# Kernel optimization log

Hardware: AMD Instinct MI355X
Metric: run time of the kernel (lower is better)

Reference implementation:

```python
import math
import jax, jax.numpy as jnp
import numpy as np

B, S, D, H, DFF = 4, 2048, 1024, 16, 4096
DK = D // H
EPS = 1e-6


def setup_inputs() -> dict:
    key = jax.random.key(0)
    ks = jax.random.split(key, 12)
    w = lambda k, sh: jax.random.normal(k, sh, dtype=jnp.float32) * 0.02
    return {
        "x": jax.random.normal(ks[0], (B, S, D), dtype=jnp.float32),
        "mask": jax.random.randint(ks[1], (B, 1, S, S), 0, 2, dtype=jnp.int32),
        "ln1_a": jnp.ones((D,), jnp.float32), "ln1_b": jnp.zeros((D,), jnp.float32),
        "Wq": w(ks[2], (D, D)), "bq": jnp.zeros((D,), jnp.float32),
        "Wk": w(ks[3], (D, D)), "bk": jnp.zeros((D,), jnp.float32),
        "Wv": w(ks[4], (D, D)), "bv": jnp.zeros((D,), jnp.float32),
        "Wo": w(ks[5], (D, D)), "bo": jnp.zeros((D,), jnp.float32),
        "ln2_a": jnp.ones((D,), jnp.float32), "ln2_b": jnp.zeros((D,), jnp.float32),
        "W1": w(ks[6], (D, DFF)), "b1": jnp.zeros((DFF,), jnp.float32),
        "W2": w(ks[7], (DFF, D)), "b2": jnp.zeros((D,), jnp.float32),
    }


def layernorm(x, a, b):
    # BERT4REC LayerNorm: unbiased std (ddof=1), eps added to std (not var)
    mean = jnp.mean(x, axis=-1, keepdims=True)
    std = jnp.std(x, axis=-1, keepdims=True, ddof=1)
    return a * (x - mean) / (std + EPS) + b


def gelu_tanh(x):
    c = math.sqrt(2.0 / math.pi)
    return 0.5 * x * (1.0 + jnp.tanh(c * (x + 0.044715 * x * x * x)))


def reference(x, mask, ln1_a, ln1_b, Wq, bq, Wk, bk, Wv, bv, Wo, bo,
              ln2_a, ln2_b, W1, b1, W2, b2):
    xb = layernorm(x, ln1_a, ln1_b)
    # multi-head attention (dropout off / eval mode)
    q = (xb @ Wq + bq).reshape(B, S, H, DK).transpose(0, 2, 1, 3)
    k = (xb @ Wk + bk).reshape(B, S, H, DK).transpose(0, 2, 1, 3)
    v = (xb @ Wv + bv).reshape(B, S, H, DK).transpose(0, 2, 1, 3)
    scores = jnp.einsum("bhqd,bhkd->bhqk", q, k) / math.sqrt(DK)
    scores = jnp.where(mask == 0, jnp.float32(-1e9), scores)
    p = jax.nn.softmax(scores, axis=-1)
    attn = jnp.einsum("bhqk,bhkd->bhqd", p, v)
    attn = attn.transpose(0, 2, 1, 3).reshape(B, S, D)
    x = x + (attn @ Wo + bo)
    # FFN sublayer
    xb = layernorm(x, ln2_a, ln2_b)
    ff = gelu_tanh(xb @ W1 + b1) @ W2 + b2
    return x + ff
```

## Files before the change

kernel.cpp:

```cpp
#include <hip/hip_runtime.h>

#define Bb 4
#define Ss 2048
#define Dd 1024
#define Hh 16
#define DFF 4096

typedef unsigned short u16;
typedef __attribute__((ext_vector_type(8))) short v8s;
typedef __attribute__((ext_vector_type(4))) float v4f;
typedef __attribute__((ext_vector_type(4))) unsigned short v4u16;
typedef __attribute__((ext_vector_type(4))) unsigned v4u;

__device__ __forceinline__ u16 f2bf(float f) {
  unsigned u = __builtin_bit_cast(unsigned, f);
  return (u16)((u + 0x7fffu + ((u >> 16) & 1u)) >> 16);
}

__device__ __forceinline__ unsigned cvtpk(float a, float b) {
  unsigned r;
  asm("v_cvt_pk_bf16_f32 %0, %1, %2" : "=v"(r) : "v"(a), "v"(b));
  return r;
}

__device__ __forceinline__ void gload16(const void* g, void* l) {
  __builtin_amdgcn_global_load_lds((const __attribute__((address_space(1))) unsigned*)g,
                                   (__attribute__((address_space(3))) unsigned*)l, 16, 0, 0);
}

__device__ __forceinline__ v4f mfma16(v8s a, v8s b, v4f c) {
  return __builtin_amdgcn_mfma_f32_16x16x32_bf16(a, b, c, 0, 0, 0);
}

__device__ __forceinline__ float gelu_f(float x) {
  float y = 0.7978845608028654f * (x + 0.044715f * x * x * x);
  y = fminf(fmaxf(y, -15.f), 15.f);
  float t = 1.0f - 2.0f / (__expf(2.0f * y) + 1.0f);
  return 0.5f * x * (1.0f + t);
}

__global__ __launch_bounds__(256)
void ln_k(const float* __restrict__ x, const float* __restrict__ ga,
          const float* __restrict__ gb, u16* __restrict__ out) {
  const int row = blockIdx.x, tid = threadIdx.x;
  const float4 v = ((const float4*)(x + (size_t)row * 1024))[tid];
  float s = v.x + v.y + v.z + v.w;
  float q = v.x * v.x + v.y * v.y + v.z * v.z + v.w * v.w;
  #pragma unroll
  for (int o = 1; o < 64; o <<= 1) { s += __shfl_xor(s, o); q += __shfl_xor(q, o); }
  __shared__ float red[8];
  if ((tid & 63) == 0) { red[tid >> 6] = s; red[4 + (tid >> 6)] = q; }
  __syncthreads();
  s = red[0] + red[1] + red[2] + red[3];
  q = red[4] + red[5] + red[6] + red[7];
  const float mean = s * (1.0f / 1024.0f);
  const float var = fmaxf((q - 1024.0f * mean * mean) * (1.0f / 1023.0f), 0.0f);
  const float inv = 1.0f / (sqrtf(var) + 1e-6f);
  const int c0 = tid * 4;
  u16* o4 = out + (size_t)row * 1024 + c0;
  const float vv[4] = {v.x, v.y, v.z, v.w};
  #pragma unroll
  for (int i = 0; i < 4; i++)
    o4[i] = f2bf(ga[c0 + i] * (vv[i] - mean) * inv + gb[c0 + i]);
}

__global__ __launch_bounds__(256)
void wt_k(const float* __restrict__ w, u16* __restrict__ wt, int K, int N) {
  __shared__ float tile[32 * 33];
  const int t = threadIdx.x;
  const int k0 = blockIdx.x << 5, n0 = blockIdx.y << 5;
  {
    const int r = t >> 3, c4 = (t & 7) << 2;
    const float4 v = *(const float4*)&w[(size_t)(k0 + r) * N + n0 + c4];
    tile[r * 33 + c4 + 0] = v.x; tile[r * 33 + c4 + 1] = v.y;
    tile[r * 33 + c4 + 2] = v.z; tile[r * 33 + c4 + 3] = v.w;
  }
  __syncthreads();
  {
    const int r = t >> 3, c4 = (t & 7) << 2;
    v4u16 uv;
    #pragma unroll
    for (int i = 0; i < 4; i++) uv[i] = f2bf(tile[(c4 + i) * 33 + r]);
    *(v4u16*)&wt[(size_t)(n0 + r) * K + k0 + c4] = uv;
  }
}

__global__ void bcat_k(const float* bq, const float* bk, const float* bv, float* dst) {
  int i = blockIdx.x * 256 + threadIdx.x;
  dst[i] = i < 1024 ? bq[i] : (i < 2048 ? bk[i - 1024] : bv[i - 2048]);
}

__global__ __launch_bounds__(256)
void mask_k(const int* __restrict__ mask, unsigned* __restrict__ mw) {
  const size_t w = (size_t)blockIdx.x * 256 + threadIdx.x;
  const int4* p = (const int4*)(mask + w * 32);
  unsigned bits = 0;
  #pragma unroll
  for (int k = 0; k < 8; k++) {
    const int4 v = p[k];
    bits |= (v.x != 0 ? 1u : 0u) << (k * 4 + 0);
    bits |= (v.y != 0 ? 1u : 0u) << (k * 4 + 1);
    bits |= (v.z != 0 ? 1u : 0u) << (k * 4 + 2);
    bits |= (v.w != 0 ? 1u : 0u) << (k * 4 + 3);
  }
  mw[w] = bits;
}

__global__ __launch_bounds__(256)
void vt_k(const u16* __restrict__ qkv, u16* __restrict__ vt) {
  __shared__ __align__(16) u16 tile[64 * 72];
  const int t = threadIdx.x;
  const int bh = blockIdx.y, b = bh >> 4, h = bh & 15;
  const size_t s0 = (size_t)blockIdx.x * 64;
  {
    const int row = t >> 2, c0 = (t & 3) << 4;
    const u16* src = &qkv[((size_t)b * Ss + s0 + row) * 3072 + 2048 + h * 64 + c0];
    *(v8s*)&tile[row * 72 + c0] = *(const v8s*)src;
    *(v8s*)&tile[row * 72 + c0 + 8] = *(const v8s*)(src + 8);
  }
  __syncthreads();
  {
    const int dk = t >> 2, sc0 = (t & 3) << 4;
    u16* dst = &vt[((size_t)bh * 64 + dk) * Ss + s0 + sc0];
    v4u16 a, bvv, cvv, d;
    #pragma unroll
    for (int i = 0; i < 4; i++) a[i] = tile[(sc0 + i) * 72 + dk];
    #pragma unroll
    for (int i = 0; i < 4; i++) bvv[i] = tile[(sc0 + 4 + i) * 72 + dk];
    #pragma unroll
    for (int i = 0; i < 4; i++) cvv[i] = tile[(sc0 + 8 + i) * 72 + dk];
    #pragma unroll
    for (int i = 0; i < 4; i++) d[i] = tile[(sc0 + 12 + i) * 72 + dk];
    *(v4u16*)(dst + 0) = a; *(v4u16*)(dst + 4) = bvv;
    *(v4u16*)(dst + 8) = cvv; *(v4u16*)(dst + 12) = d;
  }
}

template<int EPI>
__global__ __launch_bounds__(256)
void gemm_bt(const u16* __restrict__ A, const u16* __restrict__ Bt,
             const float* __restrict__ bias, const float* res,
             void* out, int M, int N, int K) {
  __shared__ __align__(16) u16 lA[2][128 * 32];
  __shared__ __align__(16) u16 lB[2][128 * 32];
  const int tid = threadIdx.x;
  const int lane = tid & 63, wid = tid >> 6;
  const int c = lane & 15, g = lane >> 4;
  const int nt = N >> 7;
  const int nwg = gridDim.x;
  const int bid0 = blockIdx.x;
  const int bid = (bid0 & 7) * (nwg >> 3) + (bid0 >> 3);
  const int bm = bid / nt, bn = bid - bm * nt;
  const int row0 = bm << 7, col0 = bn << 7;
  const int wr = (wid >> 1) << 6, wc = (wid & 1) << 6;

  v4f acc[4][4] = {};

  const int arow = tid >> 2, ak = (tid & 3) << 3;
  const u16* gA = A + (size_t)(row0 + arow) * K + ak;
  const u16* gB = Bt + (size_t)(col0 + arow) * K + ak;
  const int ldo = wid * 512;
  const size_t rstep = (size_t)64 * K;

  for (int kt = 0; kt < K; kt += 64) {
    __syncthreads();
    #pragma unroll
    for (int s = 0; s < 2; s++) {
      const int ks = kt + s * 32;
      gload16(gA + ks, &lA[s][ldo]);
      gload16(gA + ks + rstep, &lA[s][ldo + 2048]);
      gload16(gB + ks, &lB[s][ldo]);
      gload16(gB + ks + rstep, &lB[s][ldo + 2048]);
    }
    __syncthreads();
    #pragma unroll
    for (int s = 0; s < 2; s++) {
      v8s af[4], bfr[4];
      #pragma unroll
      for (int m = 0; m < 4; m++) af[m] = *(const v8s*)&lA[s][(wr + m * 16 + c) * 32 + g * 8];
      #pragma unroll
      for (int n = 0; n < 4; n++) bfr[n] = *(const v8s*)&lB[s][(wc + n * 16 + c) * 32 + g * 8];
      #pragma unroll
      for (int m = 0; m < 4; m++)
        #pragma unroll
        for (int n = 0; n < 4; n++)
          acc[m][n] = mfma16(af[m], bfr[n], acc[m][n]);
    }
  }

  float bv[4];
  #pragma unroll
  for (int n = 0; n < 4; n++) bv[n] = bias[col0 + wc + n * 16 + c];
  #pragma unroll
  for (int m = 0; m < 4; m++) {
    #pragma unroll
    for (int n = 0; n < 4; n++) {
      #pragma unroll
      for (int j = 0; j < 4; j++) {
        const int r = row0 + wr + m * 16 + g * 4 + j;
        const int cc = col0 + wc + n * 16 + c;
        const size_t idx = (size_t)r * N + cc;
        const float v = acc[m][n][j] + bv[n];
        if constexpr (EPI == 0) ((u16*)out)[idx] = f2bf(v);
        else if constexpr (EPI == 1) ((float*)out)[idx] = res[idx] + v;
        else ((u16*)out)[idx] = f2bf(gelu_f(v));
      }
    }
  }
}

__global__ __launch_bounds__(256, 4)
void attn_k(const u16* __restrict__ qkv, const u16* __restrict__ vt,
            const unsigned* __restrict__ mw, u16* __restrict__ ctx) {
  __shared__ __align__(16) u16 lK[128 * 64];
  __shared__ __align__(16) u16 lV[64 * 128];

  const int tid = threadIdx.x, lane = tid & 63, wid = tid >> 6;
  const int c = lane & 15, g = lane >> 4;
  const bool b4 = (lane & 16) != 0;
  const int bid = blockIdx.x;
  const int swz = (bid & 7) * 128 + (bid >> 3);
  const int bh = swz >> 4, qb = swz & 15;
  const int b = bh >> 4, h = bh & 15;
  const int qw = (qb << 7) + wid * 32;

  v8s qs[2][2];
  #pragma unroll
  for (int m = 0; m < 2; m++)
    #pragma unroll
    for (int ks = 0; ks < 2; ks++) {
      const v8s q = *(const v8s*)&qkv[((size_t)b * Ss + qw + m * 16 + c) * 3072 + h * 64 + ks * 32 + g * 8];
      v4u w;
      #pragma unroll
      for (int p = 0; p < 4; p++) {
        const float a = __builtin_bit_cast(float, (unsigned)((u16)q[2 * p]) << 16) * 0.18033688f;
        const float e = __builtin_bit_cast(float, (unsigned)((u16)q[2 * p + 1]) << 16) * 0.18033688f;
        w[p] = cvtpk(a, e);
      }
      qs[m][ks] = __builtin_bit_cast(v8s, w);
    }

  v4f o[2][4] = {};
  float ls[2] = {0.f, 0.f};

  const unsigned* mrow0 = mw + ((size_t)b * Ss + qw + c) * 64;

  const int skey = tid >> 3;
  const int kchunk = (((tid & 7) ^ ((tid >> 3) & 7)) << 3);
  const int vdk = tid >> 4;
  const int vchunk = (((tid & 15) ^ ((tid >> 4) & 15)) << 3);
  const u16* gK = &qkv[((size_t)b * Ss + skey) * 3072 + 1024 + h * 64 + kchunk];
  const u16* gV = &vt[((size_t)bh * 64 + vdk) * Ss + vchunk];
  u16* const dK = &lK[(wid * 8) * 64];
  u16* const dV = &lV[(wid * 4) * 128];

  for (int kt = 0; kt < 16; kt++) {
    __syncthreads();
    #pragma unroll
    for (int i = 0; i < 4; i++) {
      gload16(gK + ((size_t)kt * 128 + i * 32) * 3072, dK + i * (32 * 64));
      gload16(gV + (size_t)(i * 16) * Ss + kt * 128, dV + i * (16 * 128));
    }
    __syncthreads();

    #pragma unroll
    for (int m = 0; m < 2; m++) {
      v4f sc[8] = {};
      #pragma unroll
      for (int f = 0; f < 8; f++) {
        const v8s k0 = *(const v8s*)&lK[(f * 16 + c) * 64 + ((g ^ (c & 7)) << 3)];
        const v8s k1 = *(const v8s*)&lK[(f * 16 + c) * 64 + (((g + 4) ^ (c & 7)) << 3)];
        sc[f] = mfma16(k0, qs[m][0], sc[f]);
        sc[f] = mfma16(k1, qs[m][1], sc[f]);
      }
      const uint4 mv = *(const uint4*)(mrow0 + (size_t)m * 16 * 64 + kt * 4);
      const unsigned mvw[4] = {mv.x, mv.y, mv.z, mv.w};
      float rs = 0.f;
      #pragma unroll
      for (int f = 0; f < 8; f++) {
        const unsigned bits = mvw[f >> 1] >> (((f & 1) << 4) + (g << 2));
        #pragma unroll
        for (int j = 0; j < 4; j++) {
          float p = exp2f(fminf(sc[f][j], 30.0f));
          p = ((bits >> j) & 1u) ? p : 0.0f;
          sc[f][j] = p;
          rs += p;
        }
      }
      rs += __shfl_xor(rs, 16);
      rs += __shfl_xor(rs, 32);
      ls[m] += rs;
      unsigned p0[8], p1[8];
      #pragma unroll
      for (int f = 0; f < 8; f++) {
        p0[f] = cvtpk(sc[f][0], sc[f][1]);
        p1[f] = cvtpk(sc[f][2], sc[f][3]);
      }
      #pragma unroll
      for (int kk = 0; kk < 4; kk++) {
        unsigned X0 = p0[2 * kk],     X1 = p1[2 * kk];
        unsigned Y0 = p0[2 * kk + 1], Y1 = p1[2 * kk + 1];
        asm("v_permlane32_swap_b32 %0, %1" : "+v"(Y0), "+v"(X0));
        asm("v_permlane32_swap_b32 %0, %1" : "+v"(Y1), "+v"(X1));
        const unsigned A0 = b4 ? (unsigned)__shfl_xor((int)Y0, 16) : X0;
        const unsigned A1 = b4 ? (unsigned)__shfl_xor((int)Y1, 16) : X1;
        const unsigned B0 = b4 ? Y0 : (unsigned)__shfl_xor((int)X0, 16);
        const unsigned B1 = b4 ? Y1 : (unsigned)__shfl_xor((int)X1, 16);
        uint4 t4; t4.x = A0; t4.y = A1; t4.z = B0; t4.w = B1;
        const v8s a8 = __builtin_bit_cast(v8s, t4);
        #pragma unroll
        for (int n = 0; n < 4; n++) {
          const v8s vb = *(const v8s*)&lV[(n * 16 + c) * 128 + (((kk * 4 + g) ^ c) << 3)];
          o[m][n] = mfma16(a8, vb, o[m][n]);
        }
      }
    }
  }

  #pragma unroll
  for (int m = 0; m < 2; m++) {
    #pragma unroll
    for (int j = 0; j < 4; j++) {
      const float lsj = __shfl(ls[m], (g << 2) + j);
      const float inv = lsj > 0.f ? 1.0f / lsj : 0.f;
      const size_t row = (size_t)b * Ss + qw + m * 16 + (g << 2) + j;
      #pragma unroll
      for (int n = 0; n < 4; n++)
        ctx[row * Dd + h * 64 + n * 16 + c] = f2bf(o[m][n][j] * inv);
    }
  }
}

extern "C" void kernel_launch(void* const* d_in, const int* in_sizes, int n_in,
                              void* d_out, int out_size, void* d_ws, size_t ws_size,
                              hipStream_t stream) {
  const float* x    = (const float*)d_in[0];
  const int*   mask = (const int*)d_in[1];
  const float* ln1a = (const float*)d_in[2];
  const float* ln1b = (const float*)d_in[3];
  const float* Wq   = (const float*)d_in[4];
  const float* bq   = (const float*)d_in[5];
  const float* Wk   = (const float*)d_in[6];
  const float* bk   = (const float*)d_in[7];
  const float* Wv   = (const float*)d_in[8];
  const float* bv   = (const float*)d_in[9];
  const float* Wo   = (const float*)d_in[10];
  const float* bo   = (const float*)d_in[11];
  const float* ln2a = (const float*)d_in[12];
  const float* ln2b = (const float*)d_in[13];
  const float* W1   = (const float*)d_in[14];
  const float* b1   = (const float*)d_in[15];
  const float* W2   = (const float*)d_in[16];
  const float* b2   = (const float*)d_in[17];
  float* out = (float*)d_out;

  char* ws = (char*)d_ws;
  u16* wqkvT    = (u16*)(ws);
  u16* woT      = (u16*)(ws + 6291456);
  u16* w1T      = (u16*)(ws + 8388608);
  u16* w2T      = (u16*)(ws + 16777216);
  float* bqkv   = (float*)(ws + 25165824);
  unsigned* mw  = (unsigned*)(ws + 25178112);
  u16* xb       = (u16*)(ws + 27275264);
  u16* qkv      = (u16*)(ws + 44052480);
  u16* h1       = qkv;
  u16* vt       = (u16*)(ws + 111161344);
  u16* ctx      = (u16*)(ws + 127938560);

  wt_k<<<dim3(32, 32),  256, 0, stream>>>(Wq, wqkvT,           1024, 1024);
  wt_k<<<dim3(32, 32),  256, 0, stream>>>(Wk, wqkvT + 1048576, 1024, 1024);
  wt_k<<<dim3(32, 32),  256, 0, stream>>>(Wv, wqkvT + 2097152, 1024, 1024);
  wt_k<<<dim3(32, 32),  256, 0, stream>>>(Wo, woT,             1024, 1024);
  wt_k<<<dim3(32, 128), 256, 0, stream>>>(W1, w1T,             1024, 4096);
  wt_k<<<dim3(128, 32), 256, 0, stream>>>(W2, w2T,             4096, 1024);
  bcat_k<<<12, 256, 0, stream>>>(bq, bk, bv, bqkv);
  mask_k<<<2048, 256, 0, stream>>>(mask, mw);
  ln_k<<<8192, 256, 0, stream>>>(x, ln1a, ln1b, xb);

  gemm_bt<0><<<64 * 24, 256, 0, stream>>>(xb, wqkvT, bqkv, nullptr, qkv, 8192, 3072, 1024);
  vt_k<<<dim3(32, 64), 256, 0, stream>>>(qkv, vt);
  attn_k<<<1024, 256, 0, stream>>>(qkv, vt, mw, ctx);
  gemm_bt<1><<<64 * 8, 256, 0, stream>>>(ctx, woT, bo, x, out, 8192, 1024, 1024);
  ln_k<<<8192, 256, 0, stream>>>(out, ln2a, ln2b, xb);
  gemm_bt<2><<<64 * 32, 256, 0, stream>>>(xb, w1T, b1, nullptr, h1, 8192, 4096, 1024);
  gemm_bt<1><<<64 * 8, 256, 0, stream>>>(h1, w2T, b2, out, out, 8192, 1024, 4096);
}
```

Measured before the change: 535.0 us.

## Triple-buffer GEMM LDS stages to overlap global loads with MFMA

Replaces the load-all-then-compute loop in gemm_bt with a three-buffer software pipeline over 32-wide K slices. Global-to-LDS loads for slice t+2 are issued before computing slice t, and partial vmcnt waits with one barrier per slice replace the two full syncs per 64-wide step. This is meant to hide global memory latency behind the matrix ops. It raises LDS use to 48KB per block, which may reduce occupancy, and it depends on the manual waitcnt counts matching gload16's issue pattern.

```diff
diff --git a/kernel.cpp b/kernel.cpp
--- a/kernel.cpp
+++ b/kernel.cpp
@@ -141,8 +141,8 @@
 void gemm_bt(const u16* __restrict__ A, const u16* __restrict__ Bt,
              const float* __restrict__ bias, const float* res,
              void* out, int M, int N, int K) {
-  __shared__ __align__(16) u16 lA[2][128 * 32];
-  __shared__ __align__(16) u16 lB[2][128 * 32];
+  __shared__ __align__(16) u16 lA[3][128 * 32];
+  __shared__ __align__(16) u16 lB[3][128 * 32];
   const int tid = threadIdx.x;
   const int lane = tid & 63, wid = tid >> 6;
   const int c = lane & 15, g = lane >> 4;
@@ -161,30 +161,41 @@
   const u16* gB = Bt + (size_t)(col0 + arow) * K + ak;
   const int ldo = wid * 512;
   const size_t rstep = (size_t)64 * K;
-
-  for (int kt = 0; kt < K; kt += 64) {
-    __syncthreads();
-    #pragma unroll
-    for (int s = 0; s < 2; s++) {
-      const int ks = kt + s * 32;
-      gload16(gA + ks, &lA[s][ldo]);
-      gload16(gA + ks + rstep, &lA[s][ldo + 2048]);
-      gload16(gB + ks, &lB[s][ldo]);
-      gload16(gB + ks + rstep, &lB[s][ldo + 2048]);
-    }
-    __syncthreads();
-    #pragma unroll
-    for (int s = 0; s < 2; s++) {
-      v8s af[4], bfr[4];
-      #pragma unroll
-      for (int m = 0; m < 4; m++) af[m] = *(const v8s*)&lA[s][(wr + m * 16 + c) * 32 + g * 8];
-      #pragma unroll
-      for (int n = 0; n < 4; n++) bfr[n] = *(const v8s*)&lB[s][(wc + n * 16 + c) * 32 + g * 8];
-      #pragma unroll
-      for (int m = 0; m < 4; m++)
-        #pragma unroll
-        for (int n = 0; n < 4; n++)
-          acc[m][n] = mfma16(af[m], bfr[n], acc[m][n]);
+  const int NT = K >> 5;
+
+  auto stage = [&](int t) {
+    const int buf = t % 3;
+    const int ks = t << 5;
+    gload16(gA + ks, &lA[buf][ldo]);
+    gload16(gA + ks + rstep, &lA[buf][ldo + 2048]);
+    gload16(gB + ks, &lB[buf][ldo]);
+    gload16(gB + ks + rstep, &lB[buf][ldo + 2048]);
+  };
+
+  stage(0);
+  stage(1);
+  asm volatile("s_waitcnt vmcnt(4)" ::: "memory");
+  __builtin_amdgcn_s_barrier();
+  asm volatile("" ::: "memory");
+
+  for (int t = 0; t < NT; t++) {
+    const int buf = t % 3;
+    if (t + 2 < NT) stage(t + 2);
+    v8s af[4], bfr[4];
+    #pragma unroll
+    for (int m = 0; m < 4; m++) af[m] = *(const v8s*)&lA[buf][(wr + m * 16 + c) * 32 + g * 8];
+    #pragma unroll
+    for (int n = 0; n < 4; n++) bfr[n] = *(const v8s*)&lB[buf][(wc + n * 16 + c) * 32 + g * 8];
+    #pragma unroll
+    for (int m = 0; m < 4; m++)
+      #pragma unroll
+      for (int n = 0; n < 4; n++)
+        acc[m][n] = mfma16(af[m], bfr[n], acc[m][n]);
+    if (t + 1 < NT) {
+      if (t + 2 < NT) asm volatile("s_waitcnt vmcnt(4)" ::: "memory");
+      else            asm volatile("s_waitcnt vmcnt(0)" ::: "memory");
+      __builtin_amdgcn_s_barrier();
+      asm volatile("" ::: "memory");
     }
   }
 
```

After: 536.6 us. Within noise of the previous version (+0.3%).
